# Kernel optimization log

Measured on AMD Instinct MI355X. Metric: run time of the kernel, lower is better.

The kernel has to match this reference:

```python
import jax, jax.numpy as jnp
import numpy as np

B, N = 32, 512
NFEAT, NHID, NCLASS, NHEADS = 128, 64, 128, 8
WORK_D, SUB_D = 32, 32
H1, H2, OUT_D = 256, 256, 512
ALPHA = 0.2
NEG = -9e15


def setup_inputs() -> dict:
    key = jax.random.key(0)
    ks = jax.random.split(key, 16)
    return {
        "graph_inf": jax.random.normal(ks[0], (B, N, NFEAT), jnp.float32),
        "graph_matrix": jax.random.randint(ks[1], (B, N, N), 0, 2, jnp.int32),
        "masks": jnp.ones((B, N), jnp.float32),
        "node_order": jax.random.randint(ks[2], (B,), 0, N, jnp.int64),
        "work": jax.random.normal(ks[3], (B, WORK_D), jnp.float32),
        "subtask": jax.random.normal(ks[4], (B, SUB_D), jnp.float32),
        # GAT head params
        "W_heads": jax.random.normal(ks[5], (NHEADS, NFEAT, NHID), jnp.float32) * 0.1,
        "a_heads": jax.random.normal(ks[6], (NHEADS, 2 * NHID), jnp.float32) * 0.1,
        "W_out": jax.random.normal(ks[7], (NHID * NHEADS, NCLASS), jnp.float32) * 0.05,
        "a_out": jax.random.normal(ks[8], (2 * NCLASS,), jnp.float32) * 0.1,
        # MLP encoder params
        "fc1_w": jax.random.normal(ks[9], (NCLASS + WORK_D + SUB_D, H1), jnp.float32) * 0.07,
        "fc1_b": jnp.zeros((H1,), jnp.float32),
        "fc2_w": jax.random.normal(ks[10], (H1, H2), jnp.float32) * 0.06,
        "fc2_b": jnp.zeros((H2,), jnp.float32),
        "fc3_w": jax.random.normal(ks[11], (H2, OUT_D), jnp.float32) * 0.06,
        "fc3_b": jnp.zeros((OUT_D,), jnp.float32),
    }


def _gat_layer(Wh, a1, a2, adj, masks):
    # Wh: [B,N,F]; additive GAT score e_ij = leakyrelu(a1.Wh_i + a2.Wh_j)
    s1 = Wh @ a1  # [B,N]
    s2 = Wh @ a2  # [B,N]
    e = jax.nn.leaky_relu(s1[:, :, None] + s2[:, None, :], ALPHA)  # [B,N,N]
    att = jax.nn.softmax(jnp.where(adj > 0, e, NEG), axis=2)
    h_prime = jnp.einsum('bnm,bmf->bnf', att, Wh)
    return h_prime * masks[:, :, None]


def reference(graph_inf, graph_matrix, masks, node_order, work, subtask,
              W_heads, a_heads, W_out, a_out,
              fc1_w, fc1_b, fc2_w, fc2_b, fc3_w, fc3_b):
    adj = graph_matrix
    # multi-head GAT layer (concat=True -> ELU)
    def head(Wk, ak):
        Wh = jnp.einsum('bnf,fo->bno', graph_inf, Wk)
        return jax.nn.elu(_gat_layer(Wh, ak[:NHID], ak[NHID:], adj, masks))
    xh = jax.vmap(head)(W_heads, a_heads)  # [H,B,N,NHID]
    x = jnp.transpose(xh, (1, 2, 0, 3)).reshape(B, N, NHEADS * NHID)
    # output GAT layer (concat=False)
    Wh = jnp.einsum('bnf,fo->bno', x, W_out)
    x = _gat_layer(Wh, a_out[:NCLASS], a_out[NCLASS:], adj, masks)
    x = x * masks[:, :, None]
    # select subtask node per batch element
    selected = x[jnp.arange(B), node_order]  # [B,NCLASS]
    inf = jnp.concatenate([selected, work, subtask], axis=1)
    h = jax.nn.relu(inf @ fc1_w + fc1_b)
    h = jax.nn.relu(h @ fc2_w + fc2_b)
    out = h @ fc3_w + fc3_b
    return jax.nn.softmax(out, axis=-1)
```

## Files before the change

kernel.cpp:

```cpp
#include <hip/hip_runtime.h>

typedef unsigned short u16;
typedef unsigned int u32;
typedef unsigned long long u64;

typedef __bf16 bf16x8 __attribute__((ext_vector_type(8)));
typedef float f32x4 __attribute__((ext_vector_type(4)));

#define LOG2E 1.44269504088896340736f

__device__ __forceinline__ float b2f(u16 u) {
    u32 x = ((u32)u) << 16;
    return __builtin_bit_cast(float, x);
}
__device__ __forceinline__ u16 f2b(float f) {
    u32 u = __builtin_bit_cast(u32, f);
    u32 r = (u + 0x7fffu + ((u >> 16) & 1u)) >> 16;
    return (u16)r;
}
__device__ __forceinline__ float ld(const void* p, int i, bool bf) {
    return bf ? b2f(((const u16*)p)[i]) : ((const float*)p)[i];
}
__device__ __forceinline__ bool detect_bf16(const void* masks) {
    return ((const u16*)masks)[0] != 0;
}
__device__ __forceinline__ f32x4 mfma16(bf16x8 a, bf16x8 b, f32x4 c) {
    return __builtin_amdgcn_mfma_f32_16x16x32_bf16(a, b, c, 0, 0, 0);
}

__device__ __attribute__((aligned(256))) u32  g_adjm[16384 * 16];
__device__ __attribute__((aligned(256))) u16  g_BT1[512 * 128];
__device__ __attribute__((aligned(256))) u16  g_BT2[128 * 512];
__device__ __attribute__((aligned(256))) u16  g_Xc[32 * 512 * 128];
__device__ __attribute__((aligned(256))) u16  g_Wh1[512 * 16384];
__device__ __attribute__((aligned(256))) u16  g_xb[16384 * 512];
__device__ __attribute__((aligned(256))) u16  g_Wh2[16384 * 128];
__device__ __attribute__((aligned(256))) float g_s1a[131072];
__device__ __attribute__((aligned(256))) float g_s2a[131072];
__device__ __attribute__((aligned(256))) float g_s1b[16384];
__device__ __attribute__((aligned(256))) float g_s2b[16384];
__device__ __attribute__((aligned(256))) u16  g_fc1T[256 * 192];
__device__ __attribute__((aligned(256))) u16  g_fc2T[256 * 256];
__device__ __attribute__((aligned(256))) u16  g_fc3T[512 * 256];
__device__ __attribute__((aligned(256))) u16  g_Ahi[32 * 192];
__device__ __attribute__((aligned(256))) u16  g_Alo[32 * 192];
__device__ __attribute__((aligned(256))) u16  g_H1hi[32 * 256];
__device__ __attribute__((aligned(256))) u16  g_H1lo[32 * 256];
__device__ __attribute__((aligned(256))) u16  g_H2hi[32 * 256];
__device__ __attribute__((aligned(256))) u16  g_H2lo[32 * 256];
__device__ __attribute__((aligned(256))) float g_logits[32 * 512];

__global__ __launch_bounds__(256) void prep_kernel(
    const int* __restrict__ adj, const void* __restrict__ Whd,
    const void* __restrict__ Wo, const void* __restrict__ Xin,
    const void* __restrict__ fc1w, const void* __restrict__ fc2w,
    const void* __restrict__ fc3w, const void* __restrict__ masks)
{
    const bool bf = detect_bf16(masks);
    const int blk = blockIdx.x;
    const int tid = threadIdx.x;
    if (blk < 1024) {
        int id = blk * 256 + tid;
        int row = id >> 4, w = id & 15;
        const int4* p = (const int4*)(adj + row * 512 + w * 32);
        int4 v[8];
        #pragma unroll
        for (int s = 0; s < 8; ++s) v[s] = p[s];
        u32 word = 0;
        #pragma unroll
        for (int s = 0; s < 8; ++s) {
            u32 nib = (v[s].x > 0 ? 1u : 0u) | (v[s].y > 0 ? 2u : 0u) |
                      (v[s].z > 0 ? 4u : 0u) | (v[s].w > 0 ? 8u : 0u);
            word |= nib << (4 * s);
        }
        g_adjm[id] = word;
    } else if (blk < 1028) {
        int base = (blk - 1024) * 16384;
        for (int e = base + tid; e < base + 16384; e += 256) {
            int n = e >> 7, k = e & 127;
            g_BT1[e] = f2b(ld(Whd, (n >> 6) * 8192 + k * 64 + (n & 63), bf));
        }
    } else if (blk < 1032) {
        int base = (blk - 1028) * 16384;
        for (int e = base + tid; e < base + 16384; e += 256) {
            int n = e >> 9, k = e & 511;
            g_BT2[e] = f2b(ld(Wo, k * 128 + n, bf));
        }
    } else if (blk < 1288) {
        if (!bf) {
            int base = (blk - 1032) * 8192;
            for (int e = base + tid; e < base + 8192; e += 256)
                g_Xc[e] = f2b(((const float*)Xin)[e]);
        }
    } else if (blk < 1294) {
        int base = (blk - 1288) * 8192;
        for (int e = base + tid; e < base + 8192; e += 256) {
            int n = e / 192, k = e - n * 192;
            g_fc1T[e] = f2b(ld(fc1w, k * 256 + n, bf));
        }
    } else if (blk < 1302) {
        int base = (blk - 1294) * 8192;
        for (int e = base + tid; e < base + 8192; e += 256) {
            int n = e >> 8, k = e & 255;
            g_fc2T[e] = f2b(ld(fc2w, k * 256 + n, bf));
        }
    } else {
        int base = (blk - 1302) * 8192;
        for (int e = base + tid; e < base + 8192; e += 256) {
            int n = e >> 8, k = e & 255;
            g_fc3T[e] = f2b(ld(fc3w, k * 512 + n, bf));
        }
    }
}

__global__ __launch_bounds__(256, 2) void gemm1_kernel(
    const void* __restrict__ Xin, const void* __restrict__ a_heads,
    const void* __restrict__ masks)
{
    __shared__ __attribute__((aligned(16))) u16 Asl[128 * 72];
    __shared__ __attribute__((aligned(16))) u16 Bsl[128 * 72];
    const bool bf = detect_bf16(masks);
    const u16* Bsrc = bf ? (const u16*)Xin : g_Xc;
    const int tid = threadIdx.x;
    const int wave = tid >> 6, lane = tid & 63;
    const int wr = wave >> 1, wc = wave & 1;
    const int c = lane & 15, q = lane >> 4;
    const int tm = blockIdx.x * 128, tn = blockIdx.y * 128;
    const int srow = tid >> 1, sh = (tid & 1) * 32;
    f32x4 acc[4][4] = {};
    for (int kc = 0; kc < 128; kc += 64) {
        __syncthreads();
        const u16* Ag = g_BT1 + (tm + srow) * 128 + kc + sh;
        const u16* Bg = Bsrc + (tn + srow) * 128 + kc + sh;
        #pragma unroll
        for (int s = 0; s < 4; ++s) {
            *(uint4*)&Asl[srow * 72 + sh + 8 * s] = *(const uint4*)(Ag + 8 * s);
            *(uint4*)&Bsl[srow * 72 + sh + 8 * s] = *(const uint4*)(Bg + 8 * s);
        }
        __syncthreads();
        #pragma unroll
        for (int kt = 0; kt < 2; ++kt) {
            bf16x8 af[4], bfr[4];
            #pragma unroll
            for (int rt = 0; rt < 4; ++rt)
                af[rt] = *(const bf16x8*)&Asl[(wr * 64 + rt * 16 + c) * 72 + kt * 32 + q * 8];
            #pragma unroll
            for (int ct = 0; ct < 4; ++ct)
                bfr[ct] = *(const bf16x8*)&Bsl[(wc * 64 + ct * 16 + c) * 72 + kt * 32 + q * 8];
            #pragma unroll
            for (int rt = 0; rt < 4; ++rt)
                #pragma unroll
                for (int ct = 0; ct < 4; ++ct)
                    acc[rt][ct] = mfma16(af[rt], bfr[ct], acc[rt][ct]);
        }
    }
    #pragma unroll
    for (int rt = 0; rt < 4; ++rt)
        #pragma unroll
        for (int ct = 0; ct < 4; ++ct)
            #pragma unroll
            for (int i = 0; i < 4; ++i) {
                int r = tm + wr * 64 + rt * 16 + q * 4 + i;
                int col = tn + wc * 64 + ct * 16 + c;
                g_Wh1[r * 16384 + col] = f2b(acc[rt][ct][i]);
            }
    const int hh = blockIdx.x * 2 + wr;
    const int b = tn >> 9;
    const int nbase = (tn & 511) + wc * 64;
    float a1v[4][4], a2v[4][4];
    #pragma unroll
    for (int rt = 0; rt < 4; ++rt)
        #pragma unroll
        for (int i = 0; i < 4; ++i) {
            int o = rt * 16 + q * 4 + i;
            a1v[rt][i] = ld(a_heads, hh * 128 + o, bf);
            a2v[rt][i] = ld(a_heads, hh * 128 + 64 + o, bf);
        }
    #pragma unroll
    for (int ct = 0; ct < 4; ++ct) {
        float p1 = 0.f, p2 = 0.f;
        #pragma unroll
        for (int rt = 0; rt < 4; ++rt)
            #pragma unroll
            for (int i = 0; i < 4; ++i) {
                p1 += acc[rt][ct][i] * a1v[rt][i];
                p2 += acc[rt][ct][i] * a2v[rt][i];
            }
        p1 += __shfl_xor(p1, 16); p1 += __shfl_xor(p1, 32);
        p2 += __shfl_xor(p2, 16); p2 += __shfl_xor(p2, 32);
        if (lane < 16) {
            int n = nbase + ct * 16 + lane;
            g_s1a[(b * 8 + hh) * 512 + n] = p1 * LOG2E;
            g_s2a[(b * 8 + hh) * 512 + n] = p2 * LOG2E;
        }
    }
}

__global__ __launch_bounds__(1024, 1) void att1_kernel(const void* __restrict__ masks)
{
    __shared__ float E2s[512];
    __shared__ float E2ps[512];

    const bool bf = detect_bf16(masks);
    const int tid = threadIdx.x;
    const int w = tid >> 6, lane = tid & 63;
    const int c = lane & 15, q = lane >> 4;
    const int h  = blockIdx.x & 7;
    const int b  = blockIdx.x >> 3;

    {
        int j = tid & 511;
        float s2v = g_s2a[(b * 8 + h) * 512 + j];
        if (tid < 512) E2s[j] = exp2f(s2v);
        else           E2ps[j] = exp2f(0.2f * s2v);
    }
    __syncthreads();

    const u32* adjb = g_adjm + b * 8192;
    const u16* wt = g_Wh1 + (u32)(h * 64) * 16384 + b * 512;

    const u32 bword = (c == 0) ? 0x3F803F80u : 0u;
    const uint4 bq = {bword, bword, bword, bword};
    const bf16x8 bone = __builtin_bit_cast(bf16x8, bq);

    const int row0 = w * 32 + c;
    const int row1 = row0 + 16;
    const float s1r0 = g_s1a[(b * 8 + h) * 512 + row0];
    const float s1r1 = g_s1a[(b * 8 + h) * 512 + row1];
    const float E1_0 = exp2f(s1r0), E1p_0 = exp2f(0.2f * s1r0);
    const float E1_1 = exp2f(s1r1), E1p_1 = exp2f(0.2f * s1r1);

    f32x4 acc[2][4] = {};
    f32x4 acc1[2] = {};

    for (int kc = 0; kc < 4; ++kc) {
        union { uint4 v; u32 a[4]; } wq0, wq1;
        wq0.v = *(const uint4*)(adjb + row0 * 16 + kc * 4);
        wq1.v = *(const uint4*)(adjb + row1 * 16 + kc * 4);
        #pragma unroll
        for (int tl = 0; tl < 4; ++tl) {
            const int base = kc * 128 + tl * 32 + q * 8;
            union { float4 v[2]; float f[8]; } e2r, e2pr;
            e2r.v[0]  = *(const float4*)&E2s[base];
            e2r.v[1]  = *(const float4*)&E2s[base + 4];
            e2pr.v[0] = *(const float4*)&E2ps[base];
            e2pr.v[1] = *(const float4*)&E2ps[base + 4];
            bf16x8 bfrag[4];
            #pragma unroll
            for (int nt = 0; nt < 4; ++nt)
                bfrag[nt] = *(const bf16x8*)(wt + (u32)(nt * 16 + c) * 16384 + base);
            #pragma unroll
            for (int g = 0; g < 2; ++g) {
                const float E1  = g ? E1_1  : E1_0;
                const float E1p = g ? E1p_1 : E1p_0;
                u32 wbits = (g ? wq1.a[tl] : wq0.a[tl]) >> (q * 8);
                u32 pk[4];
                #pragma unroll
                for (int pi = 0; pi < 4; ++pi) {
                    float p0  = E1 * e2r.f[2 * pi];
                    float pp0 = E1p * e2pr.f[2 * pi];
                    float z0 = p0 > 1.f ? p0 : pp0;
                    z0 = ((wbits >> (2 * pi)) & 1u) ? z0 : 0.f;
                    float p1  = E1 * e2r.f[2 * pi + 1];
                    float pp1 = E1p * e2pr.f[2 * pi + 1];
                    float z1 = p1 > 1.f ? p1 : pp1;
                    z1 = ((wbits >> (2 * pi + 1)) & 1u) ? z1 : 0.f;
                    pk[pi] = __builtin_amdgcn_perm(__builtin_bit_cast(u32, z1),
                                                   __builtin_bit_cast(u32, z0),
                                                   0x07060302u);
                }
                uint4 pkv = {pk[0], pk[1], pk[2], pk[3]};
                bf16x8 pv = __builtin_bit_cast(bf16x8, pkv);
                acc1[g] = mfma16(pv, bone, acc1[g]);
                #pragma unroll
                for (int nt = 0; nt < 4; ++nt)
                    acc[g][nt] = mfma16(pv, bfrag[nt], acc[g][nt]);
            }
        }
    }
    #pragma unroll
    for (int g = 0; g < 2; ++g) {
        const int R = w * 32 + g * 16;
        #pragma unroll
        for (int i = 0; i < 4; ++i) {
            float lr = __shfl(acc1[g][i], (lane & 48));
            float invr = (lr == 0.f) ? (1.f / 512.f) : (1.f / lr);
            const int row = R + q * 4 + i;
            float mk = ld(masks, b * 512 + row, bf);
            #pragma unroll
            for (int nt = 0; nt < 4; ++nt) {
                float v = acc[g][nt][i] * invr * mk;
                float o = v > 0.f ? v : (__expf(v) - 1.f);
                g_xb[(b * 512 + row) * 512 + h * 64 + nt * 16 + c] = f2b(o);
            }
        }
    }
}

__global__ __launch_bounds__(256, 2) void gemm2_kernel(
    const void* __restrict__ a_out, const void* __restrict__ masks)
{
    __shared__ __attribute__((aligned(16))) u16 Asl[64 * 72];
    __shared__ __attribute__((aligned(16))) u16 Bsl[128 * 72];
    const int tid = threadIdx.x;
    const int w = tid >> 6, lane = tid & 63;
    const int c = lane & 15, q = lane >> 4;
    const int tm = blockIdx.x * 64;
    const int rowA = tid >> 2, shA = (tid & 3) * 16;
    const int rowB = tid >> 1, shB = (tid & 1) * 32;
    f32x4 acc[8] = {};
    for (int kc = 0; kc < 512; kc += 64) {
        __syncthreads();
        const u16* Ag = g_xb + (tm + rowA) * 512 + kc + shA;
        *(uint4*)&Asl[rowA * 72 + shA] = *(const uint4*)Ag;
        *(uint4*)&Asl[rowA * 72 + shA + 8] = *(const uint4*)(Ag + 8);
        const u16* Bg = g_BT2 + rowB * 512 + kc + shB;
        #pragma unroll
        for (int s = 0; s < 4; ++s)
            *(uint4*)&Bsl[rowB * 72 + shB + 8 * s] = *(const uint4*)(Bg + 8 * s);
        __syncthreads();
        #pragma unroll
        for (int kt = 0; kt < 2; ++kt) {
            bf16x8 av = *(const bf16x8*)&Asl[(w * 16 + c) * 72 + kt * 32 + q * 8];
            #pragma unroll
            for (int ct = 0; ct < 8; ++ct) {
                bf16x8 bv = *(const bf16x8*)&Bsl[(ct * 16 + c) * 72 + kt * 32 + q * 8];
                acc[ct] = mfma16(av, bv, acc[ct]);
            }
        }
    }
    const bool bf = detect_bf16(masks);
    float a1v[8], a2v[8];
    #pragma unroll
    for (int ct = 0; ct < 8; ++ct) {
        a1v[ct] = ld(a_out, ct * 16 + c, bf);
        a2v[ct] = ld(a_out, 128 + ct * 16 + c, bf);
    }
    #pragma unroll
    for (int i = 0; i < 4; ++i) {
        float p1 = 0.f, p2 = 0.f;
        #pragma unroll
        for (int ct = 0; ct < 8; ++ct) {
            p1 += acc[ct][i] * a1v[ct];
            p2 += acc[ct][i] * a2v[ct];
        }
        #pragma unroll
        for (int off = 1; off < 16; off <<= 1) {
            p1 += __shfl_xor(p1, off);
            p2 += __shfl_xor(p2, off);
        }
        if (c == 0) {
            int m = tm + w * 16 + q * 4 + i;
            g_s1b[m] = p1 * LOG2E;
            g_s2b[m] = p2 * LOG2E;
        }
    }
    #pragma unroll
    for (int ct = 0; ct < 8; ++ct)
        #pragma unroll
        for (int i = 0; i < 4; ++i) {
            int m = tm + w * 16 + q * 4 + i;
            g_Wh2[m * 128 + ct * 16 + c] = f2b(acc[ct][i]);
        }
}

__global__ __launch_bounds__(256) void fin_att(
    const void* __restrict__ masks, const int* __restrict__ node_order,
    const void* __restrict__ workv, const void* __restrict__ subtaskv)
{
    __shared__ float att[512];
    __shared__ float parts[16][128];
    __shared__ float redl[4];

    const bool bf = detect_bf16(masks);
    const int b = blockIdx.x, t = threadIdx.x;
    const int lane = t & 63, wv = t >> 6;
    const int istar = node_order[b];

    const float s1v = g_s1b[b * 512 + istar];
    const u32* arow = g_adjm + (b * 512 + istar) * 16;
    float ssum = 0.f;
    #pragma unroll
    for (int rep = 0; rep < 2; ++rep) {
        int j = t + rep * 256;
        float e = s1v + g_s2b[b * 512 + j];
        e = fmaxf(e, 0.2f * e);
        float ex = ((arow[j >> 5] >> (j & 31)) & 1u) ? exp2f(e) : 0.f;
        att[j] = ex;
        ssum += ex;
    }
    for (int off = 1; off < 64; off <<= 1) ssum += __shfl_xor(ssum, off);
    if (lane == 0) redl[wv] = ssum;
    __syncthreads();
    float tot = redl[0] + redl[1] + redl[2] + redl[3];
    bool uni = (tot == 0.f);
    float inv = uni ? (1.f / 512.f) : (1.f / tot);

    const int og = t & 15, jg = t >> 4;
    float acc[8] = {};
    const u16* base = g_Wh2 + (b * 512 + jg * 32) * 128 + og * 8;
    #pragma unroll 8
    for (int j0 = 0; j0 < 32; ++j0) {
        float wgt = uni ? 1.f : att[jg * 32 + j0];
        union { u16 u[8]; uint4 v; } z;
        z.v = *(const uint4*)(base + j0 * 128);
        #pragma unroll
        for (int i = 0; i < 8; ++i) acc[i] += wgt * b2f(z.u[i]);
    }
    #pragma unroll
    for (int i = 0; i < 8; ++i) parts[jg][og * 8 + i] = acc[i];
    __syncthreads();
    float mk = ld(masks, b * 512 + istar, bf);
    if (t < 128) {
        float s = 0.f;
        #pragma unroll
        for (int jj = 0; jj < 16; ++jj) s += parts[jj][t];
        s *= inv * mk * mk;
        u16 hi = f2b(s);
        g_Ahi[b * 192 + t] = hi;
        g_Alo[b * 192 + t] = f2b(s - b2f(hi));
    } else if (t < 160) {
        g_Ahi[b * 192 + t] = bf ? ((const u16*)workv)[b * 32 + t - 128]
                                : f2b(((const float*)workv)[b * 32 + t - 128]);
        g_Alo[b * 192 + t] = 0;
    } else if (t < 192) {
        g_Ahi[b * 192 + t] = bf ? ((const u16*)subtaskv)[b * 32 + t - 160]
                                : f2b(((const float*)subtaskv)[b * 32 + t - 160]);
        g_Alo[b * 192 + t] = 0;
    }
}

template<int K, int NOUT, bool RELU>
__device__ __forceinline__ void mlp_body(
    const u16* __restrict__ Ahi, const u16* __restrict__ Alo,
    const u16* __restrict__ WT, const void* __restrict__ bias,
    u16* __restrict__ Ohi, u16* __restrict__ Olo, float* __restrict__ Of,
    const void* __restrict__ masks)
{
    const bool bf = detect_bf16(masks);
    const int t = threadIdx.x, w = t >> 6, lane = t & 63;
    const int c = lane & 15, q = lane >> 4;
    const int col = blockIdx.x * 64 + w * 16 + c;

    const u16* wp  = WT + col * K + q * 8;
    const u16* ahp = Ahi + c * K + q * 8;
    const u16* alp = Alo + c * K + q * 8;

    f32x4 acc0 = {}, acc1 = {};
    #pragma unroll
    for (int kt = 0; kt < K / 32; ++kt) {
        bf16x8 bw  = *(const bf16x8*)(wp + kt * 32);
        bf16x8 ah0 = *(const bf16x8*)(ahp + kt * 32);
        bf16x8 al0 = *(const bf16x8*)(alp + kt * 32);
        bf16x8 ah1 = *(const bf16x8*)(ahp + 16 * K + kt * 32);
        bf16x8 al1 = *(const bf16x8*)(alp + 16 * K + kt * 32);
        acc0 = mfma16(ah0, bw, acc0);
        acc0 = mfma16(al0, bw, acc0);
        acc1 = mfma16(ah1, bw, acc1);
        acc1 = mfma16(al1, bw, acc1);
    }
    float bs = ld(bias, col, bf);
    #pragma unroll
    for (int mt = 0; mt < 2; ++mt) {
        f32x4 a = mt ? acc1 : acc0;
        #pragma unroll
        for (int i = 0; i < 4; ++i) {
            int m = mt * 16 + q * 4 + i;
            float v = a[i] + bs;
            if (RELU) {
                v = fmaxf(v, 0.f);
                u16 hi = f2b(v);
                Ohi[m * NOUT + col] = hi;
                Olo[m * NOUT + col] = f2b(v - b2f(hi));
            } else {
                Of[m * NOUT + col] = v;
            }
        }
    }
}

__global__ __launch_bounds__(256) void mlp1_kernel(const void* bias, const void* masks) {
    mlp_body<192, 256, true>(g_Ahi, g_Alo, g_fc1T, bias, g_H1hi, g_H1lo, nullptr, masks);
}
__global__ __launch_bounds__(256) void mlp2_kernel(const void* bias, const void* masks) {
    mlp_body<256, 256, true>(g_H1hi, g_H1lo, g_fc2T, bias, g_H2hi, g_H2lo, nullptr, masks);
}
__global__ __launch_bounds__(256) void mlp3_kernel(const void* bias, const void* masks) {
    mlp_body<256, 512, false>(g_H2hi, g_H2lo, g_fc3T, bias, nullptr, nullptr, g_logits, masks);
}

__global__ __launch_bounds__(64) void softmax_kernel(
    const void* __restrict__ masks, void* __restrict__ out)
{
    const bool bf = detect_bf16(masks);
    const int row = blockIdx.x, lane = threadIdx.x;
    const float* lp = g_logits + row * 512 + lane * 8;
    float v[8];
    *(float4*)&v[0] = *(const float4*)lp;
    *(float4*)&v[4] = *(const float4*)(lp + 4);
    float mx = v[0];
    #pragma unroll
    for (int i = 1; i < 8; ++i) mx = fmaxf(mx, v[i]);
    for (int off = 1; off < 64; off <<= 1) mx = fmaxf(mx, __shfl_xor(mx, off));
    float e[8];
    float s = 0.f;
    #pragma unroll
    for (int i = 0; i < 8; ++i) { e[i] = __expf(v[i] - mx); s += e[i]; }
    for (int off = 1; off < 64; off <<= 1) s += __shfl_xor(s, off);
    float inv = 1.f / s;
    if (bf) {
        u16* o = (u16*)out + row * 512 + lane * 8;
        #pragma unroll
        for (int i = 0; i < 8; ++i) o[i] = f2b(e[i] * inv);
    } else {
        float* o = (float*)out + row * 512 + lane * 8;
        #pragma unroll
        for (int i = 0; i < 8; ++i) o[i] = e[i] * inv;
    }
}

extern "C" void kernel_launch(void* const* d_in, const int* in_sizes, int n_in,
                              void* d_out, int out_size, void* d_ws, size_t ws_size,
                              hipStream_t stream)
{
    const void* graph_inf    = d_in[0];
    const int*  graph_matrix = (const int*)d_in[1];
    const void* masks        = d_in[2];
    const int*  node_order   = (const int*)d_in[3];
    const void* work         = d_in[4];
    const void* subtask      = d_in[5];
    const void* W_heads      = d_in[6];
    const void* a_heads      = d_in[7];
    const void* W_out        = d_in[8];
    const void* a_out        = d_in[9];
    const void* fc1w         = d_in[10];
    const void* fc1b         = d_in[11];
    const void* fc2w         = d_in[12];
    const void* fc2b         = d_in[13];
    const void* fc3w         = d_in[14];
    const void* fc3b         = d_in[15];

    prep_kernel<<<dim3(1318), dim3(256), 0, stream>>>(graph_matrix, W_heads, W_out, graph_inf,
                                                      fc1w, fc2w, fc3w, masks);
    gemm1_kernel<<<dim3(4, 128), dim3(256), 0, stream>>>(graph_inf, a_heads, masks);
    att1_kernel<<<dim3(256), dim3(1024), 0, stream>>>(masks);
    gemm2_kernel<<<dim3(256), dim3(256), 0, stream>>>(a_out, masks);
    fin_att<<<dim3(32), dim3(256), 0, stream>>>(masks, node_order, work, subtask);
    mlp1_kernel<<<dim3(4), dim3(256), 0, stream>>>(fc1b, masks);
    mlp2_kernel<<<dim3(4), dim3(256), 0, stream>>>(fc2b, masks);
    mlp3_kernel<<<dim3(8), dim3(256), 0, stream>>>(fc3b, masks);
    softmax_kernel<<<dim3(32), dim3(64), 0, stream>>>(masks, d_out);
}
```

Baseline: 206.8 us.

## Stage Wh tile in LDS and double rows per wave in att1

The att1 kernel now preloads the per-(batch,head) 64x512 bf16 Wh slice into padded shared memory and reads MFMA B fragments from LDS instead of global memory. Block size drops from 1024 to 512 threads, and each wave handles 64 rows (4 groups), so every B fragment is reused across more rows. The leaky-relu select is replaced by an fmaxf of the two exponential branches, which is equivalent because exp2 is monotonic. The cost is about 66KB of LDS per block, more accumulator registers per thread and fewer waves to hide latency.

```diff
diff --git a/kernel.cpp b/kernel.cpp
--- a/kernel.cpp
+++ b/kernel.cpp
@@ -196,8 +196,9 @@
     }
 }
 
-__global__ __launch_bounds__(1024, 1) void att1_kernel(const void* __restrict__ masks)
-{
+__global__ __launch_bounds__(512, 1) void att1_kernel(const void* __restrict__ masks)
+{
+    __shared__ __attribute__((aligned(16))) u16 WhL[64 * 520];
     __shared__ float E2s[512];
     __shared__ float E2ps[512];
 
@@ -208,62 +209,69 @@
     const int h  = blockIdx.x & 7;
     const int b  = blockIdx.x >> 3;
 
+    const u16* wt = g_Wh1 + (u32)(h * 64) * 16384 + b * 512;
     {
-        int j = tid & 511;
-        float s2v = g_s2a[(b * 8 + h) * 512 + j];
-        if (tid < 512) E2s[j] = exp2f(s2v);
-        else           E2ps[j] = exp2f(0.2f * s2v);
+        int r = tid >> 3, seg = tid & 7;
+        const u16* src = wt + r * 16384 + seg * 64;
+        u16* dst = &WhL[r * 520 + seg * 64];
+        *(uint4*)dst = *(const uint4*)src;
+        *(uint4*)(dst + 8) = *(const uint4*)(src + 8);
+        *(uint4*)(dst + 16) = *(const uint4*)(src + 16);
+        *(uint4*)(dst + 24) = *(const uint4*)(src + 24);
+        *(uint4*)(dst + 32) = *(const uint4*)(src + 32);
+        *(uint4*)(dst + 40) = *(const uint4*)(src + 40);
+        *(uint4*)(dst + 48) = *(const uint4*)(src + 48);
+        *(uint4*)(dst + 56) = *(const uint4*)(src + 56);
+        float s2v = g_s2a[(b * 8 + h) * 512 + tid];
+        E2s[tid]  = exp2f(s2v);
+        E2ps[tid] = exp2f(0.2f * s2v);
     }
     __syncthreads();
 
     const u32* adjb = g_adjm + b * 8192;
-    const u16* wt = g_Wh1 + (u32)(h * 64) * 16384 + b * 512;
 
     const u32 bword = (c == 0) ? 0x3F803F80u : 0u;
     const uint4 bq = {bword, bword, bword, bword};
     const bf16x8 bone = __builtin_bit_cast(bf16x8, bq);
 
-    const int row0 = w * 32 + c;
-    const int row1 = row0 + 16;
-    const float s1r0 = g_s1a[(b * 8 + h) * 512 + row0];
-    const float s1r1 = g_s1a[(b * 8 + h) * 512 + row1];
-    const float E1_0 = exp2f(s1r0), E1p_0 = exp2f(0.2f * s1r0);
-    const float E1_1 = exp2f(s1r1), E1p_1 = exp2f(0.2f * s1r1);
-
-    f32x4 acc[2][4] = {};
-    f32x4 acc1[2] = {};
+    float E1[4], E1p[4];
+    #pragma unroll
+    for (int g = 0; g < 4; ++g) {
+        float s1v = g_s1a[(b * 8 + h) * 512 + w * 64 + g * 16 + c];
+        E1[g]  = exp2f(s1v);
+        E1p[g] = exp2f(0.2f * s1v);
+    }
+
+    f32x4 acc[4][4] = {};
+    f32x4 acc1[4] = {};
+    const u16* lbase = &WhL[c * 520 + q * 8];
 
     for (int kc = 0; kc < 4; ++kc) {
-        union { uint4 v; u32 a[4]; } wq0, wq1;
-        wq0.v = *(const uint4*)(adjb + row0 * 16 + kc * 4);
-        wq1.v = *(const uint4*)(adjb + row1 * 16 + kc * 4);
+        union { uint4 v; u32 a[4]; } wq[4];
+        #pragma unroll
+        for (int g = 0; g < 4; ++g)
+            wq[g].v = *(const uint4*)(adjb + (w * 64 + g * 16 + c) * 16 + kc * 4);
         #pragma unroll
         for (int tl = 0; tl < 4; ++tl) {
-            const int base = kc * 128 + tl * 32 + q * 8;
+            const int jb = kc * 128 + tl * 32 + q * 8;
             union { float4 v[2]; float f[8]; } e2r, e2pr;
-            e2r.v[0]  = *(const float4*)&E2s[base];
-            e2r.v[1]  = *(const float4*)&E2s[base + 4];
-            e2pr.v[0] = *(const float4*)&E2ps[base];
-            e2pr.v[1] = *(const float4*)&E2ps[base + 4];
+            e2r.v[0]  = *(const float4*)&E2s[jb];
+            e2r.v[1]  = *(const float4*)&E2s[jb + 4];
+            e2pr.v[0] = *(const float4*)&E2ps[jb];
+            e2pr.v[1] = *(const float4*)&E2ps[jb + 4];
             bf16x8 bfrag[4];
             #pragma unroll
             for (int nt = 0; nt < 4; ++nt)
-                bfrag[nt] = *(const bf16x8*)(wt + (u32)(nt * 16 + c) * 16384 + base);
-            #pragma unroll
-            for (int g = 0; g < 2; ++g) {
-                const float E1  = g ? E1_1  : E1_0;
-                const float E1p = g ? E1p_1 : E1p_0;
-                u32 wbits = (g ? wq1.a[tl] : wq0.a[tl]) >> (q * 8);
+                bfrag[nt] = *(const bf16x8*)(lbase + nt * 16 * 520 + kc * 128 + tl * 32);
+            #pragma unroll
+            for (int g = 0; g < 4; ++g) {
+                u32 wbits = wq[g].a[tl] >> (q * 8);
                 u32 pk[4];
                 #pragma unroll
                 for (int pi = 0; pi < 4; ++pi) {
-                    float p0  = E1 * e2r.f[2 * pi];
-                    float pp0 = E1p * e2pr.f[2 * pi];
-                    float z0 = p0 > 1.f ? p0 : pp0;
+                    float z0 = fmaxf(E1[g] * e2r.f[2 * pi],     E1p[g] * e2pr.f[2 * pi]);
+                    float z1 = fmaxf(E1[g] * e2r.f[2 * pi + 1], E1p[g] * e2pr.f[2 * pi + 1]);
                     z0 = ((wbits >> (2 * pi)) & 1u) ? z0 : 0.f;
-                    float p1  = E1 * e2r.f[2 * pi + 1];
-                    float pp1 = E1p * e2pr.f[2 * pi + 1];
-                    float z1 = p1 > 1.f ? p1 : pp1;
                     z1 = ((wbits >> (2 * pi + 1)) & 1u) ? z1 : 0.f;
                     pk[pi] = __builtin_amdgcn_perm(__builtin_bit_cast(u32, z1),
                                                    __builtin_bit_cast(u32, z0),
@@ -279,8 +287,8 @@
         }
     }
     #pragma unroll
-    for (int g = 0; g < 2; ++g) {
-        const int R = w * 32 + g * 16;
+    for (int g = 0; g < 4; ++g) {
+        const int R = w * 64 + g * 16;
         #pragma unroll
         for (int i = 0; i < 4; ++i) {
             float lr = __shfl(acc1[g][i], (lane & 48));
@@ -543,7 +551,7 @@
     prep_kernel<<<dim3(1318), dim3(256), 0, stream>>>(graph_matrix, W_heads, W_out, graph_inf,
                                                       fc1w, fc2w, fc3w, masks);
     gemm1_kernel<<<dim3(4, 128), dim3(256), 0, stream>>>(graph_inf, a_heads, masks);
-    att1_kernel<<<dim3(256), dim3(1024), 0, stream>>>(masks);
+    att1_kernel<<<dim3(256), dim3(512), 0, stream>>>(masks);
     gemm2_kernel<<<dim3(256), dim3(256), 0, stream>>>(a_out, masks);
     fin_att<<<dim3(32), dim3(256), 0, stream>>>(masks, node_order, work, subtask);
     mlp1_kernel<<<dim3(4), dim3(256), 0, stream>>>(fc1b, masks);
```

Result: faster. 192.6 us (-6.9%).
